# Kernel optimization log

Measured on AMD Instinct MI355X. Metric: run time of the kernel, lower is better.

Reference implementation:

```python
import jax, jax.numpy as jnp
import numpy as np

NUM_HEADS = 12

def quick_gelu(z):
    return z * jax.nn.sigmoid(1.702 * z)

def setup_inputs() -> dict:
    key = jax.random.key(0)
    ks = jax.random.split(key, 8)
    B, Fn, P, E, R = 16, 12, 197, 768, 8
    s = 0.02
    return {
        "x": jax.random.normal(ks[0], (B * Fn, P, E), jnp.float32),
        "in_proj_weight": jax.random.normal(ks[1], (3 * E, E), jnp.float32) * s,
        "in_proj_bias": jnp.zeros((3 * E,), jnp.float32),
        "out_proj_weight": jax.random.normal(ks[2], (E, E), jnp.float32) * s,
        "out_proj_bias": jnp.zeros((E,), jnp.float32),
        "lora_a": jax.random.normal(ks[3], (R, E), jnp.float32) * s,
        "lora_b": jax.random.normal(ks[4], (3 * E, R), jnp.float32) * s,
        "down_w": jax.random.normal(ks[5], (R, E), jnp.float32) * s,
        "down_b": jnp.zeros((R,), jnp.float32),
        "up_w": jax.random.normal(ks[6], (E, R), jnp.float32) * s,
        "up_b": jnp.zeros((E,), jnp.float32),
        "b": B, "n_f": Fn, "token_len": P, "d_v": E,
    }

def reference(x, in_proj_weight, in_proj_bias, out_proj_weight, out_proj_bias,
              lora_a, lora_b, down_w, down_b, up_w, up_b,
              b, n_f, token_len, d_v):
    bsz, tgt, E = x.shape
    h = NUM_HEADS
    hd = E // h
    scaling = float(hd) ** -0.5

    # fused qkv + LoRA delta: [bsz, tgt, 3E]
    qkv = x @ in_proj_weight.T + in_proj_bias
    qkv = qkv + (x @ lora_a.T) @ lora_b.T
    qkv = qkv.reshape(bsz, tgt, 3, h, hd).transpose(2, 0, 3, 1, 4)
    q, k, v = qkv[0], qkv[1], qkv[2]  # each [bsz, h, tgt, hd]

    # CLS-token query per frame: (b f) h p d -> b h f d  (p=0)
    q_1 = q.reshape(b, n_f, h, tgt, hd).transpose(0, 2, 1, 3, 4)[:, :, :, 0, :]

    # per-frame local attention
    attn = jax.nn.softmax((scaling * q) @ k.transpose(0, 1, 3, 2), axis=-1)
    out = (attn @ v).transpose(0, 2, 1, 3).reshape(bsz, tgt, E)
    out = out @ out_proj_weight.T + out_proj_bias

    # cross-frame kv: (b f) h p d -> b h (f p) d
    k_all = k.reshape(b, n_f, h, tgt, hd).transpose(0, 2, 1, 3, 4).reshape(b, h, n_f * tgt, hd)
    v_all = v.reshape(b, n_f, h, tgt, hd).transpose(0, 2, 1, 3, 4).reshape(b, h, n_f * tgt, hd)

    attn_1 = jax.nn.softmax((scaling * q_1) @ k_all.transpose(0, 1, 3, 2), axis=-1)
    x_1 = (attn_1 @ v_all).transpose(0, 2, 1, 3).reshape(b, n_f, E)
    x_1 = x_1 @ out_proj_weight.T + out_proj_bias

    out = out.reshape(b, n_f, token_len, d_v)
    x_0 = out[:, :, 0, :]
    x_0 = quick_gelu(x_0 @ down_w.T + down_b) @ up_w.T + up_b
    out = out.at[:, :, 0, :].set(x_0 + x_1)
    return out.reshape(b * n_f, token_len, d_v)
```

## Files before the change

### kernel.cpp

```cpp
#include <hip/hip_runtime.h>
#include <hip/hip_bf16.h>

typedef __hip_bfloat16 bf16;
typedef __attribute__((ext_vector_type(8))) short bf16x8;
typedef __attribute__((ext_vector_type(4))) float f32x4;

#define NT   37824
#define MPAD 37888
#define EDIM 768
#define N3   2304
#define TP   197
#define NB   16
#define NF   12
#define NH   12
#define HD   64
#define SCALE 0.125f
#define KALL 2364

__device__ __forceinline__ float bits2f(unsigned short u) {
    unsigned int v = ((unsigned int)u) << 16;
    return __uint_as_float(v);
}
__device__ __forceinline__ float b2f(bf16 v) { return __bfloat162float(v); }

__device__ __forceinline__ unsigned short bhi(float x) {
    union { bf16 b; unsigned short u; } cv; cv.b = __float2bfloat16(x); return cv.u;
}
__device__ __forceinline__ unsigned short blo(float x, unsigned short h) {
    float hf = __uint_as_float(((unsigned int)h) << 16);
    union { bf16 b; unsigned short u; } cv; cv.b = __float2bfloat16(x - hf); return cv.u;
}

__device__ __forceinline__ void storeC(float* p, float v) { *p = v; }
__device__ __forceinline__ void storeC(bf16* p, float v) { *p = __float2bfloat16(v); }

__device__ __forceinline__ void gload_lds16(const bf16* g, bf16* l) {
    __builtin_amdgcn_global_load_lds(
        (const __attribute__((address_space(1))) void*)g,
        (__attribute__((address_space(3))) void*)l,
        16, 0, 0);
}

__global__ __launch_bounds__(256) void lora_mid_kernel(const float* __restrict__ x,
        const float* __restrict__ la, float* __restrict__ mid) {
    int t = blockIdx.x * 4 + (threadIdx.x >> 6);
    int lane = threadIdx.x & 63;
    if (t >= NT) return;
    float acc[8];
#pragma unroll
    for (int r = 0; r < 8; r++) acc[r] = 0.f;
    const float* xr = x + (size_t)t * EDIM;
    for (int e = lane; e < EDIM; e += 64) {
        float xv = xr[e];
#pragma unroll
        for (int r = 0; r < 8; r++) acc[r] += xv * la[r * EDIM + e];
    }
#pragma unroll
    for (int r = 0; r < 8; r++) {
        float v = acc[r];
#pragma unroll
        for (int off = 32; off >= 1; off >>= 1) v += __shfl_xor(v, off, 64);
        if (lane == 0) mid[(size_t)t * 8 + r] = v;
    }
}

__global__ __launch_bounds__(256) void split_w_kernel(const float* __restrict__ w,
        bf16* __restrict__ o, int rows) {
    int idx = blockIdx.x * 256 + threadIdx.x;
    int total = rows * 192;
    if (idx >= total) return;
    int r = idx / 192, c = (idx - r * 192) * 4;
    float4 v = *reinterpret_cast<const float4*>(w + (size_t)r * 768 + c);
    ushort4 hi, lo;
    hi.x = bhi(v.x); hi.y = bhi(v.y); hi.z = bhi(v.z); hi.w = bhi(v.w);
    lo.x = blo(v.x, hi.x); lo.y = blo(v.y, hi.y); lo.z = blo(v.z, hi.z); lo.w = blo(v.w, hi.w);
    *(ushort4*)(o + (size_t)r * 1536 + c) = hi;
    *(ushort4*)(o + (size_t)r * 1536 + 768 + c) = lo;
}

template <typename OT, bool LORA>
__global__ __launch_bounds__(512, 2) void mfma_gemm_kernel(const bf16* __restrict__ A, int lda,
        const bf16* __restrict__ W, const float* __restrict__ bias,
        const float* __restrict__ mid, const float* __restrict__ lb,
        OT* __restrict__ C, int M, int N, int KV) {
    __shared__ bf16 As[2][256 * 64];
    __shared__ bf16 Bs[2][256 * 64];
    const int tid = threadIdx.x;
    const int w = tid >> 6, lane = tid & 63;
    const int lr = lane & 15, lg = lane >> 4;
    const int wr = w >> 2, wc = w & 3;

    const int gx = gridDim.x;
    const int nwg = gx * gridDim.y;
    const int flat = blockIdx.y * gx + blockIdx.x;
    const int xcd = flat & 7, loc = flat >> 3;
    const int q = nwg >> 3, rmd = nwg & 7;
    const int lid = (xcd < rmd ? xcd * (q + 1) : rmd * (q + 1) + (xcd - rmd) * q) + loc;
    const int m0 = (lid / gx) * 256, n0 = (lid % gx) * 256;

    f32x4 acc[8][4];
#pragma unroll
    for (int i = 0; i < 8; i++)
#pragma unroll
        for (int j = 0; j < 4; j++) acc[i][j] = (f32x4){0.f, 0.f, 0.f, 0.f};

    const int brs = lane >> 3;
    const int bcsw = ((lane & 7) ^ brs) << 3;

    auto STAGE = [&](bf16* dA, bf16* dB, int aO, int wO) {
#pragma unroll
        for (int j = 0; j < 4; ++j) {
            int rA = w * 32 + j * 8;
            gload_lds16(A + (size_t)(m0 + rA + brs) * lda + aO + bcsw, dA + rA * 64);
            gload_lds16(W + (size_t)(n0 + rA + brs) * 1536 + wO + bcsw, dB + rA * 64);
        }
    };

    const int nt = KV / 64;
    STAGE(&As[0][0], &Bs[0][0], 0, 0);
    {
        const int k1 = 64;
        STAGE(&As[1][0], &Bs[1][0], (k1 >= 768) ? k1 - 768 : k1, k1);
    }
    asm volatile("s_waitcnt vmcnt(8)" ::: "memory");
    __builtin_amdgcn_sched_barrier(0);
    __builtin_amdgcn_s_barrier();
    __builtin_amdgcn_sched_barrier(0);

    int cur = 0;
    for (int t = 0; t < nt; ++t) {
        const char* pA = (const char*)&As[cur][0];
        const char* pB = (const char*)&Bs[cur][0];
        bf16x8 a[4][2], b0[2][2], b1[2][2];
#pragma unroll
        for (int mf = 0; mf < 4; mf++) {
            int row = wr * 128 + mf * 16 + lr;
            int sw = (row & 7) << 4;
            a[mf][0] = *(const bf16x8*)(pA + row * 128 + ((lg * 16) ^ sw));
            a[mf][1] = *(const bf16x8*)(pA + row * 128 + ((64 + lg * 16) ^ sw));
        }
#pragma unroll
        for (int nf = 0; nf < 2; nf++) {
            int row = wc * 64 + nf * 16 + lr;
            int sw = (row & 7) << 4;
            b0[nf][0] = *(const bf16x8*)(pB + row * 128 + ((lg * 16) ^ sw));
            b0[nf][1] = *(const bf16x8*)(pB + row * 128 + ((64 + lg * 16) ^ sw));
        }
        __builtin_amdgcn_s_setprio(1);
#pragma unroll
        for (int mf = 0; mf < 4; mf++)
#pragma unroll
            for (int nf = 0; nf < 2; nf++) {
                acc[mf][nf] = __builtin_amdgcn_mfma_f32_16x16x32_bf16(a[mf][0], b0[nf][0], acc[mf][nf], 0, 0, 0);
                acc[mf][nf] = __builtin_amdgcn_mfma_f32_16x16x32_bf16(a[mf][1], b0[nf][1], acc[mf][nf], 0, 0, 0);
            }
        __builtin_amdgcn_s_setprio(0);
#pragma unroll
        for (int nf = 0; nf < 2; nf++) {
            int row = wc * 64 + (nf + 2) * 16 + lr;
            int sw = (row & 7) << 4;
            b1[nf][0] = *(const bf16x8*)(pB + row * 128 + ((lg * 16) ^ sw));
            b1[nf][1] = *(const bf16x8*)(pB + row * 128 + ((64 + lg * 16) ^ sw));
        }
        __builtin_amdgcn_s_setprio(1);
#pragma unroll
        for (int mf = 0; mf < 4; mf++)
#pragma unroll
            for (int nf = 0; nf < 2; nf++) {
                acc[mf][nf + 2] = __builtin_amdgcn_mfma_f32_16x16x32_bf16(a[mf][0], b1[nf][0], acc[mf][nf + 2], 0, 0, 0);
                acc[mf][nf + 2] = __builtin_amdgcn_mfma_f32_16x16x32_bf16(a[mf][1], b1[nf][1], acc[mf][nf + 2], 0, 0, 0);
            }
        __builtin_amdgcn_s_setprio(0);
#pragma unroll
        for (int mf = 0; mf < 4; mf++) {
            int row = wr * 128 + 64 + mf * 16 + lr;
            int sw = (row & 7) << 4;
            a[mf][0] = *(const bf16x8*)(pA + row * 128 + ((lg * 16) ^ sw));
            a[mf][1] = *(const bf16x8*)(pA + row * 128 + ((64 + lg * 16) ^ sw));
        }
        __builtin_amdgcn_s_setprio(1);
#pragma unroll
        for (int mf = 0; mf < 4; mf++)
#pragma unroll
            for (int nf = 0; nf < 2; nf++) {
                acc[4 + mf][nf + 2] = __builtin_amdgcn_mfma_f32_16x16x32_bf16(a[mf][0], b1[nf][0], acc[4 + mf][nf + 2], 0, 0, 0);
                acc[4 + mf][nf + 2] = __builtin_amdgcn_mfma_f32_16x16x32_bf16(a[mf][1], b1[nf][1], acc[4 + mf][nf + 2], 0, 0, 0);
            }
        __builtin_amdgcn_s_setprio(0);
        __builtin_amdgcn_sched_barrier(0);
        __builtin_amdgcn_s_barrier();
        __builtin_amdgcn_sched_barrier(0);
        if (t + 2 < nt) {
            const int k2 = (t + 2) * 64;
            STAGE(&As[cur][0], &Bs[cur][0],
                  (k2 >= 768) ? k2 - 768 : k2,
                  (k2 >= 1536) ? k2 - 1536 : k2);
        }
        __builtin_amdgcn_sched_barrier(0);
        __builtin_amdgcn_s_setprio(1);
#pragma unroll
        for (int mf = 0; mf < 4; mf++)
#pragma unroll
            for (int nf = 0; nf < 2; nf++) {
                acc[4 + mf][nf] = __builtin_amdgcn_mfma_f32_16x16x32_bf16(a[mf][0], b0[nf][0], acc[4 + mf][nf], 0, 0, 0);
                acc[4 + mf][nf] = __builtin_amdgcn_mfma_f32_16x16x32_bf16(a[mf][1], b0[nf][1], acc[4 + mf][nf], 0, 0, 0);
            }
        __builtin_amdgcn_s_setprio(0);
        if (t + 2 < nt) {
            asm volatile("s_waitcnt vmcnt(8)" ::: "memory");
        } else {
            asm volatile("s_waitcnt vmcnt(0)" ::: "memory");
        }
        __builtin_amdgcn_sched_barrier(0);
        __builtin_amdgcn_s_barrier();
        __builtin_amdgcn_sched_barrier(0);
        cur ^= 1;
    }
#pragma unroll
    for (int mf = 0; mf < 8; mf++) {
#pragma unroll
        for (int r = 0; r < 4; r++) {
            int m = m0 + wr * 128 + mf * 16 + lg * 4 + r;
            if (m < M) {
                float mr[8];
                if constexpr (LORA) {
                    float4 u0 = *reinterpret_cast<const float4*>(mid + (size_t)m * 8);
                    float4 u1 = *reinterpret_cast<const float4*>(mid + (size_t)m * 8 + 4);
                    mr[0] = u0.x; mr[1] = u0.y; mr[2] = u0.z; mr[3] = u0.w;
                    mr[4] = u1.x; mr[5] = u1.y; mr[6] = u1.z; mr[7] = u1.w;
                }
#pragma unroll
                for (int nf = 0; nf < 4; nf++) {
                    int n = n0 + wc * 64 + nf * 16 + lr;
                    float v = acc[mf][nf][r] + bias[n];
                    if constexpr (LORA) {
                        const float4 l0 = *reinterpret_cast<const float4*>(lb + (size_t)n * 8);
                        const float4 l1 = *reinterpret_cast<const float4*>(lb + (size_t)n * 8 + 4);
                        v += mr[0] * l0.x + mr[1] * l0.y + mr[2] * l0.z + mr[3] * l0.w
                           + mr[4] * l1.x + mr[5] * l1.y + mr[6] * l1.z + mr[7] * l1.w;
                    }
                    storeC(C + (size_t)m * N + n, v);
                }
            }
        }
    }
}

__global__ __launch_bounds__(256) void attn_kernel(const bf16* __restrict__ qkv,
        bf16* __restrict__ ao) {
    __shared__ bf16 Ks[208 * 64];
    __shared__ bf16 Vt[64 * 208];
    __shared__ bf16 Ps[4][16 * 208];
    const int bb = blockIdx.x / NH;
    const int h = blockIdx.x % NH;
    const bf16* base = qkv + (size_t)bb * TP * N3;
    const int tid = threadIdx.x;
    const int w = tid >> 6, lane = tid & 63;
    const int lr = lane & 15, lg = lane >> 4;

    for (int idx = tid; idx < 208 * 16; idx += 256) {
        int row = idx >> 4, d4 = (idx & 15) * 4;
        ushort4 v = make_ushort4(0, 0, 0, 0);
        if (row < TP)
            v = *(const ushort4*)(base + (size_t)row * N3 + EDIM + h * 64 + d4);
        *(ushort4*)((char*)Ks + ((row * 128 + d4 * 2) ^ ((row & 7) << 4))) = v;
    }
    for (int g = w; g < 52; g += 4) {
        int kk0 = g * 4;
        int d = lane;
        const bf16* vb = base + (size_t)kk0 * N3 + 2 * EDIM + h * 64 + d;
        unsigned short t0 = 0, t1 = 0, t2 = 0, t3 = 0;
        if (kk0 + 0 < TP) t0 = *(const unsigned short*)(vb);
        if (kk0 + 1 < TP) t1 = *(const unsigned short*)(vb + N3);
        if (kk0 + 2 < TP) t2 = *(const unsigned short*)(vb + 2 * N3);
        if (kk0 + 3 < TP) t3 = *(const unsigned short*)(vb + 3 * N3);
        ushort4 v; v.x = t0; v.y = t1; v.z = t2; v.w = t3;
        *(ushort4*)((char*)Vt + ((d * 416 + kk0 * 2) ^ ((d & 7) << 4))) = v;
    }
    __syncthreads();

    bf16* Pw = &Ps[w][0];

    for (int qt = w; qt < 13; qt += 4) {
        int q = qt * 16 + lr; if (q > TP - 1) q = TP - 1;
        const bf16* qp = base + (size_t)q * N3 + h * 64 + lg * 8;
        bf16x8 qa0 = *(const bf16x8*)qp;
        bf16x8 qa1 = *(const bf16x8*)(qp + 32);

        f32x4 sf[13];
#pragma unroll
        for (int f = 0; f < 13; f++) {
            int row = f * 16 + lr;
            int swz = (row & 7) << 4;
            bf16x8 kb0 = *(const bf16x8*)((const char*)Ks + ((row * 128 + lg * 16) ^ swz));
            bf16x8 kb1 = *(const bf16x8*)((const char*)Ks + ((row * 128 + 64 + lg * 16) ^ swz));
            f32x4 c = {0.f, 0.f, 0.f, 0.f};
            c = __builtin_amdgcn_mfma_f32_16x16x32_bf16(qa0, kb0, c, 0, 0, 0);
            c = __builtin_amdgcn_mfma_f32_16x16x32_bf16(qa1, kb1, c, 0, 0, 0);
            sf[f] = c;
        }

        float mx[4] = {-1e30f, -1e30f, -1e30f, -1e30f};
#pragma unroll
        for (int f = 0; f < 13; f++) {
#pragma unroll
            for (int r = 0; r < 4; r++) {
                float s = sf[f][r] * SCALE;
                if (f == 12 && lr >= 5) s = -1e30f;
                sf[f][r] = s;
                mx[r] = fmaxf(mx[r], s);
            }
        }
#pragma unroll
        for (int off = 8; off >= 1; off >>= 1) {
#pragma unroll
            for (int r = 0; r < 4; r++) mx[r] = fmaxf(mx[r], __shfl_xor(mx[r], off, 64));
        }
        float lsum[4] = {0.f, 0.f, 0.f, 0.f};
#pragma unroll
        for (int f = 0; f < 13; f++) {
#pragma unroll
            for (int r = 0; r < 4; r++) {
                float e = __expf(sf[f][r] - mx[r]);
                sf[f][r] = e;
                lsum[r] += e;
            }
        }
#pragma unroll
        for (int off = 8; off >= 1; off >>= 1) {
#pragma unroll
            for (int r = 0; r < 4; r++) lsum[r] += __shfl_xor(lsum[r], off, 64);
        }
        float inv[4];
#pragma unroll
        for (int r = 0; r < 4; r++) inv[r] = 1.f / lsum[r];

#pragma unroll
        for (int f = 0; f < 13; f++) {
#pragma unroll
            for (int r = 0; r < 4; r++) {
                int row = lg * 4 + r;
                int col = f * 16 + lr;
                *(bf16*)((char*)Pw + ((row * 416 + col * 2) ^ ((row & 7) << 4))) =
                    __float2bfloat16(sf[f][r]);
            }
        }

        f32x4 of[4];
#pragma unroll
        for (int dt = 0; dt < 4; dt++) of[dt] = (f32x4){0.f, 0.f, 0.f, 0.f};
#pragma unroll
        for (int ks = 0; ks < 7; ks++) {
            int k0 = ks * 32 + lg * 8;
            bool ok = (k0 < 208);
            bf16x8 pa = {0, 0, 0, 0, 0, 0, 0, 0};
            if (ok)
                pa = *(const bf16x8*)((const char*)Pw + ((lr * 416 + k0 * 2) ^ ((lr & 7) << 4)));
#pragma unroll
            for (int dt = 0; dt < 4; dt++) {
                bf16x8 vb = {0, 0, 0, 0, 0, 0, 0, 0};
                if (ok) {
                    int d = dt * 16 + lr;
                    vb = *(const bf16x8*)((const char*)Vt + ((d * 416 + k0 * 2) ^ ((d & 7) << 4)));
                }
                of[dt] = __builtin_amdgcn_mfma_f32_16x16x32_bf16(pa, vb, of[dt], 0, 0, 0);
            }
        }

#pragma unroll
        for (int dt = 0; dt < 4; dt++) {
#pragma unroll
            for (int r = 0; r < 4; r++) {
                int qq = qt * 16 + lg * 4 + r;
                if (qq < TP)
                    ao[((size_t)bb * TP + qq) * EDIM + h * 64 + dt * 16 + lr] =
                        __float2bfloat16(of[dt][r] * inv[r]);
            }
        }
    }
}

__global__ __launch_bounds__(256) void xattn_kernel(const bf16* __restrict__ qkv,
        float* __restrict__ x1p) {
    __shared__ float q1[NF][64];
    __shared__ bf16 Ks[128][64];
    __shared__ bf16 Vs[128][64];
    __shared__ float sc[NF][128];
    __shared__ float Oacc[NF][64];
    __shared__ float mrow[NF], lrow[NF], arow[NF];
    const int b = blockIdx.x / NH, h = blockIdx.x % NH;
    const int tid = threadIdx.x;
    for (int idx = tid; idx < NF * 64; idx += 256) {
        int f = idx >> 6, d = idx & 63;
        q1[f][d] = b2f(qkv[(size_t)((b * NF + f) * TP) * N3 + h * 64 + d]);
        Oacc[f][d] = 0.f;
    }
    if (tid < NF) { mrow[tid] = -1e30f; lrow[tid] = 0.f; }
    __syncthreads();
    const int w = tid >> 6, lane = tid & 63;
    for (int kk0 = 0; kk0 < KALL; kk0 += 128) {
        for (int idx = tid; idx < 128 * 16; idx += 256) {
            int r = idx >> 4, d4 = (idx & 15) * 4;
            int kk = kk0 + r;
            if (kk < KALL) {
                int f = kk / TP, pp = kk - f * TP;
                const bf16* src = qkv + (size_t)((b * NF + f) * TP + pp) * N3 + h * 64 + d4;
                *(ushort4*)&Ks[r][d4] = *(const ushort4*)(src + 768);
                *(ushort4*)&Vs[r][d4] = *(const ushort4*)(src + 1536);
            } else {
                ushort4 z; z.x = z.y = z.z = z.w = 0;
                *(ushort4*)&Ks[r][d4] = z;
                *(ushort4*)&Vs[r][d4] = z;
            }
        }
        __syncthreads();
        for (int idx = tid; idx < NF * 128; idx += 256) {
            int f = idx >> 7, r = idx & 127;
            float s = -1e30f;
            if (kk0 + r < KALL) {
                const bf16* kr = &Ks[r][0];
                float a = 0.f;
#pragma unroll
                for (int d2 = 0; d2 < 32; d2++) {
                    unsigned int u = *reinterpret_cast<const unsigned int*>(kr + 2 * d2);
                    a += q1[f][2 * d2] * __uint_as_float(u << 16);
                    a += q1[f][2 * d2 + 1] * __uint_as_float(u & 0xffff0000u);
                }
                s = a * SCALE;
            }
            sc[f][r] = s;
        }
        __syncthreads();
        for (int qi = 0; qi < 3; qi++) {
            int f = qi * 4 + w;
            float s0 = sc[f][lane], s1v = sc[f][lane + 64];
            float mx = fmaxf(s0, s1v);
#pragma unroll
            for (int off = 32; off >= 1; off >>= 1) mx = fmaxf(mx, __shfl_xor(mx, off, 64));
            float mold = mrow[f];
            float mnew = fmaxf(mold, mx);
            float e0 = __expf(s0 - mnew), e1 = __expf(s1v - mnew);
            float ls = e0 + e1;
#pragma unroll
            for (int off = 32; off >= 1; off >>= 1) ls += __shfl_xor(ls, off, 64);
            sc[f][lane] = e0; sc[f][lane + 64] = e1;
            if (lane == 0) {
                float alpha = __expf(mold - mnew);
                arow[f] = alpha;
                lrow[f] = lrow[f] * alpha + ls;
                mrow[f] = mnew;
            }
        }
        __syncthreads();
        for (int idx = tid; idx < NF * 64; idx += 256) {
            int f = idx >> 6, d = idx & 63;
            float o = Oacc[f][d] * arow[f];
#pragma unroll 4
            for (int r = 0; r < 128; r++)
                o += sc[f][r] * b2f(Vs[r][d]);
            Oacc[f][d] = o;
        }
        __syncthreads();
    }
    for (int idx = tid; idx < NF * 64; idx += 256) {
        int f = idx >> 6, d = idx & 63;
        x1p[(size_t)(b * NF + f) * EDIM + h * 64 + d] = Oacc[f][d] / lrow[f];
    }
}

__global__ __launch_bounds__(256) void cls_kernel(float* __restrict__ out,
        const float* __restrict__ x1p, const float* __restrict__ Wout, const float* __restrict__ ob,
        const float* __restrict__ dw, const float* __restrict__ db,
        const float* __restrict__ uw, const float* __restrict__ ub) {
    __shared__ float x0s[EDIM], x1s[EDIM], gs[8];
    const int bfi = blockIdx.x;
    float* row = out + (size_t)bfi * TP * EDIM;
    const int tid = threadIdx.x;
    for (int i = tid; i < EDIM; i += 256) {
        x0s[i] = row[i];
        x1s[i] = x1p[(size_t)bfi * EDIM + i];
    }
    __syncthreads();
    {
        int r = tid >> 5, sl = tid & 31;
        float pr = 0.f;
        for (int e = sl; e < EDIM; e += 32) pr += x0s[e] * dw[r * EDIM + e];
#pragma unroll
        for (int off = 16; off >= 1; off >>= 1) pr += __shfl_xor(pr, off, 64);
        if (sl == 0) gs[r] = pr + db[r];
    }
    __syncthreads();
    float act[8];
#pragma unroll
    for (int r = 0; r < 8; r++) { float g = gs[r]; act[r] = g / (1.f + __expf(-1.702f * g)); }
    for (int j = tid; j < EDIM; j += 256) {
        float y = ub[j] + ob[j];
        const float4 u0 = *reinterpret_cast<const float4*>(uw + (size_t)j * 8);
        const float4 u1 = *reinterpret_cast<const float4*>(uw + (size_t)j * 8 + 4);
        y += act[0] * u0.x + act[1] * u0.y + act[2] * u0.z + act[3] * u0.w
           + act[4] * u1.x + act[5] * u1.y + act[6] * u1.z + act[7] * u1.w;
        const float* wr = Wout + (size_t)j * EDIM;
        float s = 0.f;
        for (int e = 0; e < EDIM; e += 4) {
            float4 wv = *reinterpret_cast<const float4*>(wr + e);
            s += x1s[e] * wv.x + x1s[e + 1] * wv.y + x1s[e + 2] * wv.z + x1s[e + 3] * wv.w;
        }
        y += s;
        row[j] = y;
    }
}

extern "C" void kernel_launch(void* const* d_in, const int* in_sizes, int n_in,
                              void* d_out, int out_size, void* d_ws, size_t ws_size,
                              hipStream_t stream) {
    (void)in_sizes; (void)n_in; (void)out_size; (void)ws_size;
    const float* x   = (const float*)d_in[0];
    const float* ipw = (const float*)d_in[1];
    const float* ipb = (const float*)d_in[2];
    const float* opw = (const float*)d_in[3];
    const float* opb = (const float*)d_in[4];
    const float* la  = (const float*)d_in[5];
    const float* lb  = (const float*)d_in[6];
    const float* dw  = (const float*)d_in[7];
    const float* db  = (const float*)d_in[8];
    const float* uw  = (const float*)d_in[9];
    const float* ub  = (const float*)d_in[10];
    float* out = (float*)d_out;

    char* wsb = (char*)d_ws;
    bf16* qkv = (bf16*)wsb;                       wsb += (size_t)NT * N3 * sizeof(bf16);
    bf16* ao  = (bf16*)wsb;                       wsb += (size_t)MPAD * EDIM * sizeof(bf16);
    bf16* xs  = (bf16*)wsb;                       wsb += (size_t)MPAD * 1536 * sizeof(bf16);
    bf16* W1  = (bf16*)wsb;                       wsb += (size_t)N3 * 1536 * sizeof(bf16);
    bf16* W2  = (bf16*)wsb;                       wsb += (size_t)EDIM * 1536 * sizeof(bf16);
    float* mid = (float*)wsb;                     wsb += (size_t)NT * 8 * sizeof(float);
    float* x1p = (float*)wsb;                     wsb += (size_t)NB * NF * EDIM * sizeof(float);

    split_w_kernel<<<(N3 * 192 + 255) / 256, 256, 0, stream>>>(ipw, W1, N3);
    split_w_kernel<<<(EDIM * 192 + 255) / 256, 256, 0, stream>>>(opw, W2, EDIM);
    split_w_kernel<<<(NT * 192 + 255) / 256, 256, 0, stream>>>(x, xs, NT);
    lora_mid_kernel<<<NT / 4, 256, 0, stream>>>(x, la, mid);
    mfma_gemm_kernel<bf16, true><<<dim3(N3 / 256, MPAD / 256), 512, 0, stream>>>(
        xs, 1536, W1, ipb, mid, lb, qkv, NT, N3, 2304);
    attn_kernel<<<192 * NH, 256, 0, stream>>>(qkv, ao);
    xattn_kernel<<<NB * NH, 256, 0, stream>>>(qkv, x1p);
    mfma_gemm_kernel<float, false><<<dim3(EDIM / 256, MPAD / 256), 512, 0, stream>>>(
        ao, 768, W2, opb, nullptr, nullptr, out, NT, EDIM, 1536);
    cls_kernel<<<NB * NF, 256, 0, stream>>>(out, x1p, opw, opb, dw, db, uw, ub);
}
```

Baseline: 1.456 ms.

## Split cross-frame attention over key chunks and hoist Q loads in attn

The cross-frame CLS attention kernel previously ran only 192 blocks, each scanning all 2364 keys serially. It is now split into 4 key chunks per (batch, head), each producing a partial output with its running max and sum, and a new merge kernel combines them with log-sum-exp rescaling. This is meant to raise parallelism on a GPU with many CUs, at the cost of an extra launch and a small partial-result buffer. Separately, attn_kernel now loads its Q fragments into registers before the K/V shared-memory staging so the global load latency overlaps the staging, which raises register pressure.

```diff
diff --git a/kernel.cpp b/kernel.cpp
--- a/kernel.cpp
+++ b/kernel.cpp
@@ -16,6 +16,8 @@
 #define HD   64
 #define SCALE 0.125f
 #define KALL 2364
+#define NCH  4
+#define KCH  591
 
 __device__ __forceinline__ float bits2f(unsigned short u) {
     unsigned int v = ((unsigned int)u) << 16;
@@ -258,6 +260,18 @@
     const int w = tid >> 6, lane = tid & 63;
     const int lr = lane & 15, lg = lane >> 4;
 
+    bf16x8 qa[4][2];
+#pragma unroll
+    for (int ti = 0; ti < 4; ti++) {
+        int qt = w + ti * 4;
+        if (qt < 13) {
+            int q = qt * 16 + lr; if (q > TP - 1) q = TP - 1;
+            const bf16* qp = base + (size_t)q * N3 + h * 64 + lg * 8;
+            qa[ti][0] = *(const bf16x8*)qp;
+            qa[ti][1] = *(const bf16x8*)(qp + 32);
+        }
+    }
+
     for (int idx = tid; idx < 208 * 16; idx += 256) {
         int row = idx >> 4, d4 = (idx & 15) * 4;
         ushort4 v = make_ushort4(0, 0, 0, 0);
@@ -281,11 +295,10 @@
 
     bf16* Pw = &Ps[w][0];
 
-    for (int qt = w; qt < 13; qt += 4) {
-        int q = qt * 16 + lr; if (q > TP - 1) q = TP - 1;
-        const bf16* qp = base + (size_t)q * N3 + h * 64 + lg * 8;
-        bf16x8 qa0 = *(const bf16x8*)qp;
-        bf16x8 qa1 = *(const bf16x8*)(qp + 32);
+#pragma unroll
+    for (int ti = 0; ti < 4; ti++) {
+        int qt = w + ti * 4;
+        if (qt >= 13) continue;
 
         f32x4 sf[13];
 #pragma unroll
@@ -295,8 +308,8 @@
             bf16x8 kb0 = *(const bf16x8*)((const char*)Ks + ((row * 128 + lg * 16) ^ swz));
             bf16x8 kb1 = *(const bf16x8*)((const char*)Ks + ((row * 128 + 64 + lg * 16) ^ swz));
             f32x4 c = {0.f, 0.f, 0.f, 0.f};
-            c = __builtin_amdgcn_mfma_f32_16x16x32_bf16(qa0, kb0, c, 0, 0, 0);
-            c = __builtin_amdgcn_mfma_f32_16x16x32_bf16(qa1, kb1, c, 0, 0, 0);
+            c = __builtin_amdgcn_mfma_f32_16x16x32_bf16(qa[ti][0], kb0, c, 0, 0, 0);
+            c = __builtin_amdgcn_mfma_f32_16x16x32_bf16(qa[ti][1], kb1, c, 0, 0, 0);
             sf[f] = c;
         }
 
@@ -380,16 +393,20 @@
     }
 }
 
-__global__ __launch_bounds__(256) void xattn_kernel(const bf16* __restrict__ qkv,
-        float* __restrict__ x1p) {
+__global__ __launch_bounds__(256) void xattn_part_kernel(const bf16* __restrict__ qkv,
+        float* __restrict__ Opart, float* __restrict__ mlp) {
     __shared__ float q1[NF][64];
     __shared__ bf16 Ks[128][64];
     __shared__ bf16 Vs[128][64];
     __shared__ float sc[NF][128];
     __shared__ float Oacc[NF][64];
     __shared__ float mrow[NF], lrow[NF], arow[NF];
-    const int b = blockIdx.x / NH, h = blockIdx.x % NH;
+    const int bid = blockIdx.x;
+    const int c = bid & (NCH - 1);
+    const int bh = bid >> 2;
+    const int b = bh / NH, h = bh % NH;
     const int tid = threadIdx.x;
+    const int kbeg = c * KCH, kend = kbeg + KCH;
     for (int idx = tid; idx < NF * 64; idx += 256) {
         int f = idx >> 6, d = idx & 63;
         q1[f][d] = b2f(qkv[(size_t)((b * NF + f) * TP) * N3 + h * 64 + d]);
@@ -398,11 +415,11 @@
     if (tid < NF) { mrow[tid] = -1e30f; lrow[tid] = 0.f; }
     __syncthreads();
     const int w = tid >> 6, lane = tid & 63;
-    for (int kk0 = 0; kk0 < KALL; kk0 += 128) {
+    for (int kk0 = kbeg; kk0 < kend; kk0 += 128) {
         for (int idx = tid; idx < 128 * 16; idx += 256) {
             int r = idx >> 4, d4 = (idx & 15) * 4;
             int kk = kk0 + r;
-            if (kk < KALL) {
+            if (kk < kend) {
                 int f = kk / TP, pp = kk - f * TP;
                 const bf16* src = qkv + (size_t)((b * NF + f) * TP + pp) * N3 + h * 64 + d4;
                 *(ushort4*)&Ks[r][d4] = *(const ushort4*)(src + 768);
@@ -417,7 +434,7 @@
         for (int idx = tid; idx < NF * 128; idx += 256) {
             int f = idx >> 7, r = idx & 127;
             float s = -1e30f;
-            if (kk0 + r < KALL) {
+            if (kk0 + r < kend) {
                 const bf16* kr = &Ks[r][0];
                 float a = 0.f;
 #pragma unroll
@@ -464,7 +481,34 @@
     }
     for (int idx = tid; idx < NF * 64; idx += 256) {
         int f = idx >> 6, d = idx & 63;
-        x1p[(size_t)(b * NF + f) * EDIM + h * 64 + d] = Oacc[f][d] / lrow[f];
+        Opart[((size_t)bid * NF + f) * 64 + d] = Oacc[f][d];
+    }
+    if (tid < NF) {
+        mlp[(size_t)bid * NF * 2 + tid] = mrow[tid];
+        mlp[(size_t)bid * NF * 2 + NF + tid] = lrow[tid];
+    }
+}
+
+__global__ __launch_bounds__(256) void xattn_merge_kernel(const float* __restrict__ Opart,
+        const float* __restrict__ mlp, float* __restrict__ x1p) {
+    const int bh = blockIdx.x;
+    const int b = bh / NH, h = bh % NH;
+    const int tid = threadIdx.x;
+    for (int idx = tid; idx < NF * 64; idx += 256) {
+        int f = idx >> 6, d = idx & 63;
+        float M = -1e30f;
+#pragma unroll
+        for (int c = 0; c < NCH; c++)
+            M = fmaxf(M, mlp[(size_t)(bh * NCH + c) * NF * 2 + f]);
+        float L = 0.f, O = 0.f;
+#pragma unroll
+        for (int c = 0; c < NCH; c++) {
+            int pb = bh * NCH + c;
+            float s = __expf(mlp[(size_t)pb * NF * 2 + f] - M);
+            L += mlp[(size_t)pb * NF * 2 + NF + f] * s;
+            O += Opart[((size_t)pb * NF + f) * 64 + d] * s;
+        }
+        x1p[(size_t)(b * NF + f) * EDIM + h * 64 + d] = O / L;
     }
 }
 
@@ -535,6 +579,8 @@
     bf16* W2  = (bf16*)wsb;                       wsb += (size_t)EDIM * 1536 * sizeof(bf16);
     float* mid = (float*)wsb;                     wsb += (size_t)NT * 8 * sizeof(float);
     float* x1p = (float*)wsb;                     wsb += (size_t)NB * NF * EDIM * sizeof(float);
+    float* Opart = (float*)wsb;                   wsb += (size_t)NB * NH * NCH * NF * 64 * sizeof(float);
+    float* mlp = (float*)wsb;                     wsb += (size_t)NB * NH * NCH * NF * 2 * sizeof(float);
 
     split_w_kernel<<<(N3 * 192 + 255) / 256, 256, 0, stream>>>(ipw, W1, N3);
     split_w_kernel<<<(EDIM * 192 + 255) / 256, 256, 0, stream>>>(opw, W2, EDIM);
@@ -543,7 +589,8 @@
     mfma_gemm_kernel<bf16, true><<<dim3(N3 / 256, MPAD / 256), 512, 0, stream>>>(
         xs, 1536, W1, ipb, mid, lb, qkv, NT, N3, 2304);
     attn_kernel<<<192 * NH, 256, 0, stream>>>(qkv, ao);
-    xattn_kernel<<<NB * NH, 256, 0, stream>>>(qkv, x1p);
+    xattn_part_kernel<<<NB * NH * NCH, 256, 0, stream>>>(qkv, Opart, mlp);
+    xattn_merge_kernel<<<NB * NH, 256, 0, stream>>>(Opart, mlp, x1p);
     mfma_gemm_kernel<float, false><<<dim3(EDIM / 256, MPAD / 256), 512, 0, stream>>>(
         ao, 768, W2, opb, nullptr, nullptr, out, NT, EDIM, 1536);
     cls_kernel<<<NB * NF, 256, 0, stream>>>(out, x1p, opw, opb, dw, db, uw, ub);
```

After: 1.266 ms. 13.1% less time.
